# Optimization experiments

Hardware: AMD Instinct MI355X
Metric: run time of the kernel (lower is better)

The kernel has to match this reference:

```python
import jax, jax.numpy as jnp
import numpy as np

N, C, K, STEPS = 131072, 256, 5, 20


def setup_inputs() -> dict:
    key = jax.random.key(0)
    k1, k2, k3, k4 = jax.random.split(key, 4)
    drive = jax.random.uniform(k1, (N, C), dtype=jnp.float32)  # sigmoid-like drive in [0,1]
    K_raw = jax.random.uniform(k2, (K,), dtype=jnp.float32)
    K_local = K_raw / K_raw.sum()  # positive, sums to 1
    W = jax.random.uniform(k3, (C, C), dtype=jnp.float32)
    mask = (jax.random.uniform(k4, (C, C)) < 0.2).astype(jnp.float32)
    W = W * mask
    W_cc = W / jnp.clip(W.sum(axis=0, keepdims=True), 1e-8)  # column-stochastic
    r = jnp.full((C,), 3.9, dtype=jnp.float32)
    eps = jnp.full((C,), 0.3, dtype=jnp.float32)
    beta = jnp.full((C,), 0.1, dtype=jnp.float32)
    return {"drive": drive, "r": r, "eps": eps, "beta": beta,
            "K_local": K_local, "W_cc": W_cc}


def reference(drive, r, eps, beta, K_local, W_cc):
    # readout == 'final' (module default)
    pad = K // 2
    one_m_eps = 1.0 - eps
    one_m_beta = 1.0 - beta

    def step(grid, _):
        mapped = r * grid * (1.0 - grid)  # [N, C] logistic map
        # circular conv1d over channel axis (cross-correlation, kernel K_local)
        local = K_local[0] * jnp.roll(mapped, pad, axis=-1)
        for j in range(1, K):
            local = local + K_local[j] * jnp.roll(mapped, pad - j, axis=-1)
        global_cc = mapped @ W_cc  # [N, C]
        coupled = 0.5 * (local + global_cc)
        physics = one_m_eps * mapped + eps * coupled
        new_grid = one_m_beta * physics + beta * drive
        return new_grid, None

    grid, _ = jax.lax.scan(step, drive, None, length=STEPS)
    return jnp.clip(grid, 1e-4, 1.0 - 1e-4)
```

## Files before the change

kernel.cpp:

```cpp
#include <hip/hip_runtime.h>

#define C_DIM 256
#define STEPS 20
#define ROWS_PER_WG 32

typedef _Float16 f16;
typedef f16 f16x8 __attribute__((ext_vector_type(8)));
typedef float f32x4 __attribute__((ext_vector_type(4)));

__global__ __launch_bounds__(256) void prep_w(const float* __restrict__ W,
                                              const float* __restrict__ Kl,
                                              f16* __restrict__ whi,
                                              f16* __restrict__ wlo)
{
    const int gwave = (int)(blockIdx.x * blockDim.x + threadIdx.x) >> 6;
    const int l = (int)threadIdx.x & 63;
    if (gwave >= 128) return;
    const int kb = gwave >> 4, nb = gwave & 15;
    const int n = nb * 16 + (l & 15);
    const int kbase = kb * 32 + (l >> 4) * 8;
    f16 h[8], lo[8];
    #pragma unroll
    for (int j = 0; j < 8; ++j) {
        const int k = kbase + j;
        float v = 0.5f * W[k * C_DIM + n];
        const int d = (k - n + 2) & (C_DIM - 1);
        if (d < 5) v += 0.5f * Kl[d];
        const f16 hh = (f16)v;
        h[j] = hh;
        lo[j] = (f16)((v - (float)hh) * 4096.0f);
    }
    const size_t off = (size_t)gwave * 512 + (size_t)l * 8;
    *(f16x8*)(whi + off) = *(f16x8*)h;
    *(f16x8*)(wlo + off) = *(f16x8*)lo;
}

__global__ __launch_bounds__(512, 2) void cml_main(
    const float* __restrict__ drive,
    const float* __restrict__ r_,
    const float* __restrict__ eps_,
    const float* __restrict__ beta_,
    const f16* __restrict__ whi,
    const f16* __restrict__ wlo,
    float* __restrict__ out)
{
    __shared__ char smem[65536];

    const int tid = (int)threadIdx.x;
    const int w   = tid >> 6;
    const int l   = tid & 63;
    const int kg  = l >> 4;
    const int cl  = l & 15;
    const int wcol0 = w * 32;
    const size_t rowBase = (size_t)blockIdx.x * ROWS_PER_WG;

    f16x8 Bh[8][2], Bl[8][2];
    #pragma unroll
    for (int kb = 0; kb < 8; ++kb) {
        #pragma unroll
        for (int nb = 0; nb < 2; ++nb) {
            const size_t f = (size_t)(kb * 16 + w * 2 + nb) * 512 + (size_t)l * 8;
            Bh[kb][nb] = *(const f16x8*)(whi + f);
            Bl[kb][nb] = *(const f16x8*)(wlo + f);
        }
    }

    float rr[2], P1[2], P2[2];
    float g[2][2][4], m_[2][2][4], drv[2][2][4];
    #pragma unroll
    for (int nb = 0; nb < 2; ++nb) {
        const int c = wcol0 + nb * 16 + cl;
        const float rv = r_[c], ev = eps_[c], bv = beta_[c];
        rr[nb] = rv;
        P1[nb] = (1.0f - bv) * (1.0f - ev);
        P2[nb] = (1.0f - bv) * ev;
        #pragma unroll
        for (int mb = 0; mb < 2; ++mb) {
            #pragma unroll
            for (int r = 0; r < 4; ++r) {
                const size_t row = rowBase + (size_t)(mb * 16 + kg * 4 + r);
                const float dv = drive[row * C_DIM + c];
                g[mb][nb][r]   = dv;
                drv[mb][nb][r] = bv * dv;
            }
        }
    }

    f32x4 acch[2][2], accl[2][2];
    #pragma unroll
    for (int mb = 0; mb < 2; ++mb)
        #pragma unroll
        for (int nb = 0; nb < 2; ++nb) {
            acch[mb][nb] = (f32x4)0.0f;
            accl[mb][nb] = (f32x4)0.0f;
        }

    #pragma unroll 1
    for (int s = 0; s < STEPS; ++s) {
        char* ph = smem + ((s & 1) << 15);
        char* pl = ph + 16384;

        #pragma unroll
        for (int mb = 0; mb < 2; ++mb) {
            #pragma unroll
            for (int nb = 0; nb < 2; ++nb) {
                const int chunk = (wcol0 >> 3) + nb * 2 + (cl >> 3);
                #pragma unroll
                for (int r = 0; r < 4; ++r) {
                    const float gv = g[mb][nb][r];
                    const float mv = rr[nb] * gv * (1.0f - gv);
                    m_[mb][nb][r] = mv;
                    const f16 hh = (f16)mv;
                    const f16 ll = (f16)((mv - (float)hh) * 4096.0f);
                    const int row = mb * 16 + kg * 4 + r;
                    const int off = (row << 9) + (((chunk ^ (row & 7))) << 4) + ((cl & 7) << 1);
                    *(f16*)(ph + off) = hh;
                    *(f16*)(pl + off) = ll;
                }
            }
        }
        __syncthreads();

        #pragma unroll
        for (int kb = 0; kb < 8; ++kb) {
            #pragma unroll
            for (int mb = 0; mb < 2; ++mb) {
                const int arow = mb * 16 + cl;
                const int aoff = (arow << 9) + (((kb * 4 + kg) ^ (arow & 7)) << 4);
                const f16x8 ahi = *(const f16x8*)(ph + aoff);
                const f16x8 alo = *(const f16x8*)(pl + aoff);
                #pragma unroll
                for (int nb = 0; nb < 2; ++nb) {
                    acch[mb][nb] = __builtin_amdgcn_mfma_f32_16x16x32_f16(ahi, Bh[kb][nb], acch[mb][nb], 0, 0, 0);
                    accl[mb][nb] = __builtin_amdgcn_mfma_f32_16x16x32_f16(alo, Bh[kb][nb], accl[mb][nb], 0, 0, 0);
                    accl[mb][nb] = __builtin_amdgcn_mfma_f32_16x16x32_f16(ahi, Bl[kb][nb], accl[mb][nb], 0, 0, 0);
                }
            }
        }

        #pragma unroll
        for (int mb = 0; mb < 2; ++mb) {
            #pragma unroll
            for (int nb = 0; nb < 2; ++nb) {
                #pragma unroll
                for (int r = 0; r < 4; ++r) {
                    const float coupled = acch[mb][nb][r] + accl[mb][nb][r] * (1.0f / 4096.0f);
                    g[mb][nb][r] = P1[nb] * m_[mb][nb][r] + P2[nb] * coupled + drv[mb][nb][r];
                    acch[mb][nb][r] = 0.0f;
                    accl[mb][nb][r] = 0.0f;
                }
            }
        }
    }

    #pragma unroll
    for (int mb = 0; mb < 2; ++mb) {
        #pragma unroll
        for (int nb = 0; nb < 2; ++nb) {
            const int c = wcol0 + nb * 16 + cl;
            #pragma unroll
            for (int r = 0; r < 4; ++r) {
                const size_t row = rowBase + (size_t)(mb * 16 + kg * 4 + r);
                float v = g[mb][nb][r];
                v = fminf(fmaxf(v, 1e-4f), 1.0f - 1e-4f);
                out[row * C_DIM + c] = v;
            }
        }
    }
}

extern "C" void kernel_launch(void* const* d_in, const int* in_sizes, int n_in,
                              void* d_out, int out_size, void* d_ws, size_t ws_size,
                              hipStream_t stream) {
    (void)n_in; (void)ws_size; (void)out_size;
    const float* drive = (const float*)d_in[0];
    const float* r     = (const float*)d_in[1];
    const float* eps   = (const float*)d_in[2];
    const float* beta  = (const float*)d_in[3];
    const float* Kl    = (const float*)d_in[4];
    const float* W     = (const float*)d_in[5];
    float* out = (float*)d_out;

    f16* whi = (f16*)d_ws;
    f16* wlo = whi + 65536;

    prep_w<<<dim3(32), dim3(256), 0, stream>>>(W, Kl, whi, wlo);

    const int nrows = in_sizes[0] / C_DIM;
    cml_main<<<dim3((unsigned)(nrows / ROWS_PER_WG)), dim3(512), 0, stream>>>(
        drive, r, eps, beta, whi, wlo, out);
}
```

Before: 792.8 us.

## Transpose MFMA operands so state is channel-major, enabling vector LDS writes and overlapped epilogue

Swaps the MFMA operand roles so the coupling matrix is the A operand held in registers and the state is the B operand read from LDS. Each lane then holds four consecutive channels, which allows packed f16x4 LDS stores and float4 global loads and stores. The logistic map for the next step is fused into the epilogue of the current tile, so LDS writes for step s+1 interleave with MFMA work. This also removes the separate pre-sync store phase. The cost is a more intricate XOR-swizzled addressing scheme, which risks bank conflicts or indexing errors.

```diff
diff --git a/kernel.cpp b/kernel.cpp
--- a/kernel.cpp
+++ b/kernel.cpp
@@ -5,6 +5,7 @@
 #define ROWS_PER_WG 32
 
 typedef _Float16 f16;
+typedef f16 f16x4 __attribute__((ext_vector_type(4)));
 typedef f16 f16x8 __attribute__((ext_vector_type(8)));
 typedef float f32x4 __attribute__((ext_vector_type(4)));
 
@@ -13,11 +14,11 @@
                                               f16* __restrict__ whi,
                                               f16* __restrict__ wlo)
 {
-    const int gwave = (int)(blockIdx.x * blockDim.x + threadIdx.x) >> 6;
+    const int f = (int)(blockIdx.x * blockDim.x + threadIdx.x) >> 6;
     const int l = (int)threadIdx.x & 63;
-    if (gwave >= 128) return;
-    const int kb = gwave >> 4, nb = gwave & 15;
-    const int n = nb * 16 + (l & 15);
+    if (f >= 128) return;
+    const int mt = f >> 3, kb = f & 7;
+    const int n = mt * 16 + (l & 15);
     const int kbase = kb * 32 + (l >> 4) * 8;
     f16 h[8], lo[8];
     #pragma unroll
@@ -30,7 +31,7 @@
         h[j] = hh;
         lo[j] = (f16)((v - (float)hh) * 4096.0f);
     }
-    const size_t off = (size_t)gwave * 512 + (size_t)l * 8;
+    const size_t off = (size_t)f * 512 + (size_t)l * 8;
     *(f16x8*)(whi + off) = *(f16x8*)h;
     *(f16x8*)(wlo + off) = *(f16x8*)lo;
 }
@@ -51,120 +52,146 @@
     const int l   = tid & 63;
     const int kg  = l >> 4;
     const int cl  = l & 15;
-    const int wcol0 = w * 32;
     const size_t rowBase = (size_t)blockIdx.x * ROWS_PER_WG;
 
-    f16x8 Bh[8][2], Bl[8][2];
-    #pragma unroll
-    for (int kb = 0; kb < 8; ++kb) {
-        #pragma unroll
-        for (int nb = 0; nb < 2; ++nb) {
-            const size_t f = (size_t)(kb * 16 + w * 2 + nb) * 512 + (size_t)l * 8;
-            Bh[kb][nb] = *(const f16x8*)(whi + f);
-            Bl[kb][nb] = *(const f16x8*)(wlo + f);
-        }
-    }
-
-    float rr[2], P1[2], P2[2];
+    f16x8 Wh[2][8], Wl[2][8];
+    #pragma unroll
+    for (int mti = 0; mti < 2; ++mti) {
+        #pragma unroll
+        for (int kb = 0; kb < 8; ++kb) {
+            const size_t off = (size_t)((w * 2 + mti) * 8 + kb) * 512 + (size_t)l * 8;
+            Wh[mti][kb] = *(const f16x8*)(whi + off);
+            Wl[mti][kb] = *(const f16x8*)(wlo + off);
+        }
+    }
+
+    float rr[2][4], P1[2][4], P2[2][4];
+    #pragma unroll
+    for (int mti = 0; mti < 2; ++mti) {
+        const int ch0 = (w * 2 + mti) * 16 + kg * 4;
+        #pragma unroll
+        for (int r = 0; r < 4; ++r) {
+            const int ch = ch0 + r;
+            const float rv = r_[ch], ev = eps_[ch], bv = beta_[ch];
+            rr[mti][r] = rv;
+            P1[mti][r] = (1.0f - bv) * (1.0f - ev);
+            P2[mti][r] = (1.0f - bv) * ev;
+        }
+    }
+
     float g[2][2][4], m_[2][2][4], drv[2][2][4];
     #pragma unroll
-    for (int nb = 0; nb < 2; ++nb) {
-        const int c = wcol0 + nb * 16 + cl;
-        const float rv = r_[c], ev = eps_[c], bv = beta_[c];
-        rr[nb] = rv;
-        P1[nb] = (1.0f - bv) * (1.0f - ev);
-        P2[nb] = (1.0f - bv) * ev;
-        #pragma unroll
-        for (int mb = 0; mb < 2; ++mb) {
+    for (int mti = 0; mti < 2; ++mti) {
+        const int ch0 = (w * 2 + mti) * 16 + kg * 4;
+        #pragma unroll
+        for (int nt = 0; nt < 2; ++nt) {
+            const size_t row = rowBase + (size_t)(nt * 16 + cl);
+            const f32x4 d4 = *(const f32x4*)(drive + row * C_DIM + ch0);
             #pragma unroll
             for (int r = 0; r < 4; ++r) {
-                const size_t row = rowBase + (size_t)(mb * 16 + kg * 4 + r);
-                const float dv = drive[row * C_DIM + c];
-                g[mb][nb][r]   = dv;
-                drv[mb][nb][r] = bv * dv;
-            }
-        }
-    }
-
-    f32x4 acch[2][2], accl[2][2];
-    #pragma unroll
-    for (int mb = 0; mb < 2; ++mb)
-        #pragma unroll
-        for (int nb = 0; nb < 2; ++nb) {
-            acch[mb][nb] = (f32x4)0.0f;
-            accl[mb][nb] = (f32x4)0.0f;
-        }
+                const float bv = beta_[ch0 + r];
+                g[mti][nt][r]   = d4[r];
+                drv[mti][nt][r] = bv * d4[r];
+            }
+        }
+    }
+
+    int rbase[2], woff[2][2];
+    #pragma unroll
+    for (int nt = 0; nt < 2; ++nt) {
+        const int m = nt * 16 + cl;
+        rbase[nt] = (m << 9) + (kg << 4) + ((m & 7) << 6);
+        #pragma unroll
+        for (int mti = 0; mti < 2; ++mti) {
+            const int c = (w * 2 + mti) * 2 + (kg >> 1);
+            const int p = c ^ ((m & 7) << 2);
+            woff[mti][nt] = (m << 9) + (p << 4) + ((kg & 1) << 3);
+        }
+    }
+
+    #pragma unroll
+    for (int mti = 0; mti < 2; ++mti) {
+        #pragma unroll
+        for (int nt = 0; nt < 2; ++nt) {
+            f16x4 hv, lv;
+            #pragma unroll
+            for (int r = 0; r < 4; ++r) {
+                const float gv = g[mti][nt][r];
+                const float mv = rr[mti][r] * gv * (1.0f - gv);
+                m_[mti][nt][r] = mv;
+                const f16 hh = (f16)mv;
+                hv[r] = hh;
+                lv[r] = (f16)((mv - (float)hh) * 4096.0f);
+            }
+            *(f16x4*)(smem + woff[mti][nt]) = hv;
+            *(f16x4*)(smem + woff[mti][nt] + 16384) = lv;
+        }
+    }
 
     #pragma unroll 1
     for (int s = 0; s < STEPS; ++s) {
-        char* ph = smem + ((s & 1) << 15);
-        char* pl = ph + 16384;
-
-        #pragma unroll
-        for (int mb = 0; mb < 2; ++mb) {
-            #pragma unroll
-            for (int nb = 0; nb < 2; ++nb) {
-                const int chunk = (wcol0 >> 3) + nb * 2 + (cl >> 3);
+        __syncthreads();
+        const int rb = (s & 1) << 15;
+        const int wb = rb ^ 32768;
+
+        #pragma unroll
+        for (int nt = 0; nt < 2; ++nt) {
+            f32x4 acch[2], accl[2];
+            #pragma unroll
+            for (int mti = 0; mti < 2; ++mti) {
+                acch[mti] = (f32x4)0.0f;
+                accl[mti] = (f32x4)0.0f;
+            }
+
+            const int Ab = rbase[nt] | rb;
+            #pragma unroll
+            for (int kb = 0; kb < 8; ++kb) {
+                const int addr = Ab ^ (kb << 6);
+                const f16x8 bh = *(const f16x8*)(smem + addr);
+                const f16x8 bl = *(const f16x8*)(smem + addr + 16384);
+                #pragma unroll
+                for (int mti = 0; mti < 2; ++mti) {
+                    acch[mti] = __builtin_amdgcn_mfma_f32_16x16x32_f16(Wh[mti][kb], bh, acch[mti], 0, 0, 0);
+                    accl[mti] = __builtin_amdgcn_mfma_f32_16x16x32_f16(Wl[mti][kb], bh, accl[mti], 0, 0, 0);
+                    accl[mti] = __builtin_amdgcn_mfma_f32_16x16x32_f16(Wh[mti][kb], bl, accl[mti], 0, 0, 0);
+                }
+            }
+
+            #pragma unroll
+            for (int mti = 0; mti < 2; ++mti) {
+                f16x4 hv, lv;
                 #pragma unroll
                 for (int r = 0; r < 4; ++r) {
-                    const float gv = g[mb][nb][r];
-                    const float mv = rr[nb] * gv * (1.0f - gv);
-                    m_[mb][nb][r] = mv;
+                    const float coupled = fmaf(accl[mti][r], 1.0f / 4096.0f, acch[mti][r]);
+                    const float gn = fmaf(P1[mti][r], m_[mti][nt][r],
+                                     fmaf(P2[mti][r], coupled, drv[mti][nt][r]));
+                    g[mti][nt][r] = gn;
+                    const float mv = rr[mti][r] * gn * (1.0f - gn);
+                    m_[mti][nt][r] = mv;
                     const f16 hh = (f16)mv;
-                    const f16 ll = (f16)((mv - (float)hh) * 4096.0f);
-                    const int row = mb * 16 + kg * 4 + r;
-                    const int off = (row << 9) + (((chunk ^ (row & 7))) << 4) + ((cl & 7) << 1);
-                    *(f16*)(ph + off) = hh;
-                    *(f16*)(pl + off) = ll;
+                    hv[r] = hh;
+                    lv[r] = (f16)((mv - (float)hh) * 4096.0f);
                 }
-            }
-        }
-        __syncthreads();
-
-        #pragma unroll
-        for (int kb = 0; kb < 8; ++kb) {
-            #pragma unroll
-            for (int mb = 0; mb < 2; ++mb) {
-                const int arow = mb * 16 + cl;
-                const int aoff = (arow << 9) + (((kb * 4 + kg) ^ (arow & 7)) << 4);
-                const f16x8 ahi = *(const f16x8*)(ph + aoff);
-                const f16x8 alo = *(const f16x8*)(pl + aoff);
-                #pragma unroll
-                for (int nb = 0; nb < 2; ++nb) {
-                    acch[mb][nb] = __builtin_amdgcn_mfma_f32_16x16x32_f16(ahi, Bh[kb][nb], acch[mb][nb], 0, 0, 0);
-                    accl[mb][nb] = __builtin_amdgcn_mfma_f32_16x16x32_f16(alo, Bh[kb][nb], accl[mb][nb], 0, 0, 0);
-                    accl[mb][nb] = __builtin_amdgcn_mfma_f32_16x16x32_f16(ahi, Bl[kb][nb], accl[mb][nb], 0, 0, 0);
+                if (s != STEPS - 1) {
+                    *(f16x4*)(smem + (woff[mti][nt] | wb)) = hv;
+                    *(f16x4*)(smem + (woff[mti][nt] | wb) + 16384) = lv;
                 }
             }
         }
-
-        #pragma unroll
-        for (int mb = 0; mb < 2; ++mb) {
-            #pragma unroll
-            for (int nb = 0; nb < 2; ++nb) {
-                #pragma unroll
-                for (int r = 0; r < 4; ++r) {
-                    const float coupled = acch[mb][nb][r] + accl[mb][nb][r] * (1.0f / 4096.0f);
-                    g[mb][nb][r] = P1[nb] * m_[mb][nb][r] + P2[nb] * coupled + drv[mb][nb][r];
-                    acch[mb][nb][r] = 0.0f;
-                    accl[mb][nb][r] = 0.0f;
-                }
-            }
-        }
-    }
-
-    #pragma unroll
-    for (int mb = 0; mb < 2; ++mb) {
-        #pragma unroll
-        for (int nb = 0; nb < 2; ++nb) {
-            const int c = wcol0 + nb * 16 + cl;
+    }
+
+    #pragma unroll
+    for (int mti = 0; mti < 2; ++mti) {
+        const int ch0 = (w * 2 + mti) * 16 + kg * 4;
+        #pragma unroll
+        for (int nt = 0; nt < 2; ++nt) {
+            const size_t row = rowBase + (size_t)(nt * 16 + cl);
+            f32x4 o;
             #pragma unroll
             for (int r = 0; r < 4; ++r) {
-                const size_t row = rowBase + (size_t)(mb * 16 + kg * 4 + r);
-                float v = g[mb][nb][r];
-                v = fminf(fmaxf(v, 1e-4f), 1.0f - 1e-4f);
-                out[row * C_DIM + c] = v;
-            }
+                o[r] = fminf(fmaxf(g[mti][nt][r], 1e-4f), 1.0f - 1e-4f);
+            }
+            *(f32x4*)(out + row * C_DIM + ch0) = o;
         }
     }
 }
```

New measurement: 812.2 us. 2.4% more time.

## Restructure CML kernel to transposed 32x32x16 MFMA with padded LDS and software-pipelined reads

Applied to the files above, without the earlier changes.

Switches the GEMM to compute W^T·m^T using 32x32x16 f16 MFMAs, so the weight slices stay in registers as the A operand and each wave owns 32 output channels for all 32 rows. LDS rows are padded (640-byte stride) instead of XOR-swizzled, drive*beta is parked in LDS to free registers, and B-operand LDS reads are prefetched one slice ahead with setprio around the MFMAs. The logistic map is fused into the epilogue so there is a single barrier per step, and global loads/stores are vectorized. LDS use grows to about 120KB dynamic, which likely limits occupancy to one workgroup per CU.

```diff
diff --git a/kernel.cpp b/kernel.cpp
--- a/kernel.cpp
+++ b/kernel.cpp
@@ -3,22 +3,29 @@
 #define C_DIM 256
 #define STEPS 20
 #define ROWS_PER_WG 32
+#define LDS_ROW 640
+#define PLANE 20480
+#define BUFSZ 40960
+#define DRV_OFF 81920
+#define SMEM_TOT (81920 + 512 * 80)
 
 typedef _Float16 f16;
+typedef f16 f16x4 __attribute__((ext_vector_type(4)));
 typedef f16 f16x8 __attribute__((ext_vector_type(8)));
 typedef float f32x4 __attribute__((ext_vector_type(4)));
+typedef float f32x16 __attribute__((ext_vector_type(16)));
 
 __global__ __launch_bounds__(256) void prep_w(const float* __restrict__ W,
                                               const float* __restrict__ Kl,
                                               f16* __restrict__ whi,
                                               f16* __restrict__ wlo)
 {
-    const int gwave = (int)(blockIdx.x * blockDim.x + threadIdx.x) >> 6;
+    const int f = (int)(blockIdx.x * blockDim.x + threadIdx.x) >> 6;
     const int l = (int)threadIdx.x & 63;
-    if (gwave >= 128) return;
-    const int kb = gwave >> 4, nb = gwave & 15;
-    const int n = nb * 16 + (l & 15);
-    const int kbase = kb * 32 + (l >> 4) * 8;
+    if (f >= 128) return;
+    const int mt32 = f >> 4, s = f & 15;
+    const int n = mt32 * 32 + (l & 31);
+    const int kbase = s * 16 + (l >> 5) * 8;
     f16 h[8], lo[8];
     #pragma unroll
     for (int j = 0; j < 8; ++j) {
@@ -30,7 +37,7 @@
         h[j] = hh;
         lo[j] = (f16)((v - (float)hh) * 4096.0f);
     }
-    const size_t off = (size_t)gwave * 512 + (size_t)l * 8;
+    const size_t off = (size_t)f * 512 + (size_t)l * 8;
     *(f16x8*)(whi + off) = *(f16x8*)h;
     *(f16x8*)(wlo + off) = *(f16x8*)lo;
 }
@@ -44,127 +51,138 @@
     const f16* __restrict__ wlo,
     float* __restrict__ out)
 {
-    __shared__ char smem[65536];
+    extern __shared__ char smem[];
 
     const int tid = (int)threadIdx.x;
     const int w   = tid >> 6;
     const int l   = tid & 63;
-    const int kg  = l >> 4;
-    const int cl  = l & 15;
-    const int wcol0 = w * 32;
+    const int n   = l & 31;
+    const int h   = l >> 5;
     const size_t rowBase = (size_t)blockIdx.x * ROWS_PER_WG;
-
-    f16x8 Bh[8][2], Bl[8][2];
-    #pragma unroll
-    for (int kb = 0; kb < 8; ++kb) {
-        #pragma unroll
-        for (int nb = 0; nb < 2; ++nb) {
-            const size_t f = (size_t)(kb * 16 + w * 2 + nb) * 512 + (size_t)l * 8;
-            Bh[kb][nb] = *(const f16x8*)(whi + f);
-            Bl[kb][nb] = *(const f16x8*)(wlo + f);
-        }
-    }
-
-    float rr[2], P1[2], P2[2];
-    float g[2][2][4], m_[2][2][4], drv[2][2][4];
-    #pragma unroll
-    for (int nb = 0; nb < 2; ++nb) {
-        const int c = wcol0 + nb * 16 + cl;
-        const float rv = r_[c], ev = eps_[c], bv = beta_[c];
-        rr[nb] = rv;
-        P1[nb] = (1.0f - bv) * (1.0f - ev);
-        P2[nb] = (1.0f - bv) * ev;
-        #pragma unroll
-        for (int mb = 0; mb < 2; ++mb) {
+    const int drvBase = DRV_OFF + tid * 80;
+
+    f16x8 Wh[16], Wl[16];
+    #pragma unroll
+    for (int s = 0; s < 16; ++s) {
+        const size_t off = (size_t)(w * 16 + s) * 512 + (size_t)l * 8;
+        Wh[s] = *(const f16x8*)(whi + off);
+        Wl[s] = *(const f16x8*)(wlo + off);
+    }
+
+    float rr[16], P1[16], P2[16];
+    #pragma unroll
+    for (int reg = 0; reg < 16; ++reg) {
+        const int ch = w * 32 + (reg & 3) + 8 * (reg >> 2) + 4 * h;
+        const float rv = r_[ch], ev = eps_[ch], bv = beta_[ch];
+        rr[reg] = rv;
+        P1[reg] = (1.0f - bv) * (1.0f - ev);
+        P2[reg] = (1.0f - bv) * ev;
+    }
+
+    float gm[16];
+    {
+        const size_t row = rowBase + (size_t)n;
+        #pragma unroll
+        for (int mg = 0; mg < 4; ++mg) {
+            const int ch0 = w * 32 + mg * 8 + 4 * h;
+            const f32x4 d4 = *(const f32x4*)(drive + row * C_DIM + ch0);
+            f32x4 dv;
             #pragma unroll
-            for (int r = 0; r < 4; ++r) {
-                const size_t row = rowBase + (size_t)(mb * 16 + kg * 4 + r);
-                const float dv = drive[row * C_DIM + c];
-                g[mb][nb][r]   = dv;
-                drv[mb][nb][r] = bv * dv;
-            }
-        }
-    }
-
-    f32x4 acch[2][2], accl[2][2];
-    #pragma unroll
-    for (int mb = 0; mb < 2; ++mb)
-        #pragma unroll
-        for (int nb = 0; nb < 2; ++nb) {
-            acch[mb][nb] = (f32x4)0.0f;
-            accl[mb][nb] = (f32x4)0.0f;
-        }
+            for (int e = 0; e < 4; ++e) {
+                gm[mg * 4 + e] = d4[e];
+                dv[e] = beta_[ch0 + e] * d4[e];
+            }
+            *(f32x4*)(smem + drvBase + (mg << 4)) = dv;
+        }
+    }
+
+    const int rdb = n * LDS_ROW + ((h + (n & 7)) << 4);
+    const int wrb = n * LDS_ROW + (((w << 2) + (n & 7)) << 4) + (h << 3);
+
+    #pragma unroll
+    for (int reg = 0; reg < 16; ++reg) {
+        const float gv = gm[reg];
+        gm[reg] = rr[reg] * gv * (1.0f - gv);
+    }
+    #pragma unroll
+    for (int mg = 0; mg < 4; ++mg) {
+        f16x4 hv, lv;
+        #pragma unroll
+        for (int e = 0; e < 4; ++e) {
+            const float mv = gm[mg * 4 + e];
+            const f16 hh = (f16)mv;
+            hv[e] = hh;
+            lv[e] = (f16)((mv - (float)hh) * 4096.0f);
+        }
+        *(f16x4*)(smem + wrb + (mg << 4)) = hv;
+        *(f16x4*)(smem + wrb + (mg << 4) + PLANE) = lv;
+    }
 
     #pragma unroll 1
     for (int s = 0; s < STEPS; ++s) {
-        char* ph = smem + ((s & 1) << 15);
-        char* pl = ph + 16384;
-
-        #pragma unroll
-        for (int mb = 0; mb < 2; ++mb) {
+        __syncthreads();
+        const int rb = (s & 1) * BUFSZ;
+        const int wbuf = BUFSZ - rb;
+        const char* rp = smem + rb + rdb;
+        const int lastStep = (s == STEPS - 1);
+
+        f32x16 acch = (f32x16)0.0f, accl = (f32x16)0.0f;
+
+        f16x8 bh = *(const f16x8*)(rp);
+        f16x8 bl = *(const f16x8*)(rp + PLANE);
+        #pragma unroll
+        for (int sl = 0; sl < 16; ++sl) {
+            f16x8 nbh, nbl;
+            if (sl < 15) {
+                nbh = *(const f16x8*)(rp + 32 * (sl + 1));
+                nbl = *(const f16x8*)(rp + PLANE + 32 * (sl + 1));
+            }
+            __builtin_amdgcn_s_setprio(1);
+            acch = __builtin_amdgcn_mfma_f32_32x32x16_f16(Wh[sl], bh, acch, 0, 0, 0);
+            accl = __builtin_amdgcn_mfma_f32_32x32x16_f16(Wl[sl], bh, accl, 0, 0, 0);
+            accl = __builtin_amdgcn_mfma_f32_32x32x16_f16(Wh[sl], bl, accl, 0, 0, 0);
+            __builtin_amdgcn_s_setprio(0);
+            if (sl < 15) { bh = nbh; bl = nbl; }
+        }
+
+        #pragma unroll
+        for (int mg = 0; mg < 4; ++mg) {
+            const f32x4 dv = *(const f32x4*)(smem + drvBase + (mg << 4));
+            f16x4 hv, lv;
             #pragma unroll
-            for (int nb = 0; nb < 2; ++nb) {
-                const int chunk = (wcol0 >> 3) + nb * 2 + (cl >> 3);
-                #pragma unroll
-                for (int r = 0; r < 4; ++r) {
-                    const float gv = g[mb][nb][r];
-                    const float mv = rr[nb] * gv * (1.0f - gv);
-                    m_[mb][nb][r] = mv;
+            for (int e = 0; e < 4; ++e) {
+                const int reg = mg * 4 + e;
+                const float coupled = fmaf(accl[reg], 1.0f / 4096.0f, acch[reg]);
+                const float gn = fmaf(P1[reg], gm[reg],
+                                 fmaf(P2[reg], coupled, dv[e]));
+                if (lastStep) {
+                    gm[reg] = gn;
+                } else {
+                    const float mv = rr[reg] * gn * (1.0f - gn);
+                    gm[reg] = mv;
                     const f16 hh = (f16)mv;
-                    const f16 ll = (f16)((mv - (float)hh) * 4096.0f);
-                    const int row = mb * 16 + kg * 4 + r;
-                    const int off = (row << 9) + (((chunk ^ (row & 7))) << 4) + ((cl & 7) << 1);
-                    *(f16*)(ph + off) = hh;
-                    *(f16*)(pl + off) = ll;
+                    hv[e] = hh;
+                    lv[e] = (f16)((mv - (float)hh) * 4096.0f);
                 }
             }
-        }
-        __syncthreads();
-
-        #pragma unroll
-        for (int kb = 0; kb < 8; ++kb) {
+            if (!lastStep) {
+                *(f16x4*)(smem + wbuf + wrb + (mg << 4)) = hv;
+                *(f16x4*)(smem + wbuf + wrb + (mg << 4) + PLANE) = lv;
+            }
+        }
+    }
+
+    {
+        const size_t row = rowBase + (size_t)n;
+        #pragma unroll
+        for (int mg = 0; mg < 4; ++mg) {
+            const int ch0 = w * 32 + mg * 8 + 4 * h;
+            f32x4 o;
             #pragma unroll
-            for (int mb = 0; mb < 2; ++mb) {
-                const int arow = mb * 16 + cl;
-                const int aoff = (arow << 9) + (((kb * 4 + kg) ^ (arow & 7)) << 4);
-                const f16x8 ahi = *(const f16x8*)(ph + aoff);
-                const f16x8 alo = *(const f16x8*)(pl + aoff);
-                #pragma unroll
-                for (int nb = 0; nb < 2; ++nb) {
-                    acch[mb][nb] = __builtin_amdgcn_mfma_f32_16x16x32_f16(ahi, Bh[kb][nb], acch[mb][nb], 0, 0, 0);
-                    accl[mb][nb] = __builtin_amdgcn_mfma_f32_16x16x32_f16(alo, Bh[kb][nb], accl[mb][nb], 0, 0, 0);
-                    accl[mb][nb] = __builtin_amdgcn_mfma_f32_16x16x32_f16(ahi, Bl[kb][nb], accl[mb][nb], 0, 0, 0);
-                }
-            }
-        }
-
-        #pragma unroll
-        for (int mb = 0; mb < 2; ++mb) {
-            #pragma unroll
-            for (int nb = 0; nb < 2; ++nb) {
-                #pragma unroll
-                for (int r = 0; r < 4; ++r) {
-                    const float coupled = acch[mb][nb][r] + accl[mb][nb][r] * (1.0f / 4096.0f);
-                    g[mb][nb][r] = P1[nb] * m_[mb][nb][r] + P2[nb] * coupled + drv[mb][nb][r];
-                    acch[mb][nb][r] = 0.0f;
-                    accl[mb][nb][r] = 0.0f;
-                }
-            }
-        }
-    }
-
-    #pragma unroll
-    for (int mb = 0; mb < 2; ++mb) {
-        #pragma unroll
-        for (int nb = 0; nb < 2; ++nb) {
-            const int c = wcol0 + nb * 16 + cl;
-            #pragma unroll
-            for (int r = 0; r < 4; ++r) {
-                const size_t row = rowBase + (size_t)(mb * 16 + kg * 4 + r);
-                float v = g[mb][nb][r];
-                v = fminf(fmaxf(v, 1e-4f), 1.0f - 1e-4f);
-                out[row * C_DIM + c] = v;
-            }
+            for (int e = 0; e < 4; ++e) {
+                o[e] = fminf(fmaxf(gm[mg * 4 + e], 1e-4f), 1.0f - 1e-4f);
+            }
+            *(f32x4*)(out + row * C_DIM + ch0) = o;
         }
     }
 }
@@ -186,7 +204,10 @@
 
     prep_w<<<dim3(32), dim3(256), 0, stream>>>(W, Kl, whi, wlo);
 
+    hipFuncSetAttribute((const void*)cml_main,
+                        hipFuncAttributeMaxDynamicSharedMemorySize, SMEM_TOT);
+
     const int nrows = in_sizes[0] / C_DIM;
-    cml_main<<<dim3((unsigned)(nrows / ROWS_PER_WG)), dim3(512), 0, stream>>>(
+    cml_main<<<dim3((unsigned)(nrows / ROWS_PER_WG)), dim3(512), SMEM_TOT, stream>>>(
         drive, r, eps, beta, whi, wlo, out);
 }
```

After: 916.1 us. 1.16x slower.
